# Kernel optimization log

Measured on AMD Instinct MI355X. Metric: run time of the kernel, lower is better.

## Reference

```python
import jax, jax.numpy as jnp
import numpy as np

EPS = 1e-5  # batch-norm epsilon


def subm_conv(feat, nbrs, W):
    # feat: [N, Cin], nbrs: [N, K] int indices into feat (rulebook), W: [K, Cin, Cout]
    gathered = feat[nbrs]                      # [N, K, Cin]  irregular gather
    return jnp.einsum('nkc,kcd->nd', gathered, W)


def batch_norm(f, gamma, beta):
    # training-mode BN over active sites (scn.BatchNormalization semantics)
    mean = jnp.mean(f, axis=0)
    var = jnp.var(f, axis=0)
    return (f - mean) * jax.lax.rsqrt(var + EPS) * gamma + beta


def setup_inputs() -> dict:
    key = jax.random.key(0)
    k1, k2, k3, k4 = jax.random.split(key, 4)
    N, K, C = 300000, 9, 64
    scale = 1.0 / np.sqrt(K * C)
    return {
        'x': jax.random.normal(k1, (N, C), dtype=jnp.float32),
        'nbrs': jax.random.randint(k2, (N, K), 0, N, dtype=jnp.int32),
        'W1': jax.random.normal(k3, (K, C, C), dtype=jnp.float32) * scale,
        'gamma1': jnp.ones((C,), jnp.float32),
        'beta1': jnp.zeros((C,), jnp.float32),
        'W2': jax.random.normal(k4, (K, C, C), dtype=jnp.float32) * scale,
        'gamma2': jnp.ones((C,), jnp.float32),
        'beta2': jnp.zeros((C,), jnp.float32),
    }


def reference(x, nbrs, W1, gamma1, beta1, W2, gamma2, beta2):
    residual = x
    out = subm_conv(x, nbrs, W1)                       # conv1 (no bias)
    out = jax.nn.relu(batch_norm(out, gamma1, beta1))  # BatchNormReLU
    out = subm_conv(out, nbrs, W2)                     # conv2 (no bias)
    out = batch_norm(out, gamma2, beta2)               # BatchNormalization
    out = jax.nn.relu(out + residual)                  # AddTable + ReLU
    return out
```

## Files before the change

### kernel.cpp

```cpp
#include <hip/hip_runtime.h>

#define NROWS 300000
#define NBLK ((NROWS + 63) / 64)

typedef float f32x4 __attribute__((ext_vector_type(4)));
typedef short s16x8 __attribute__((ext_vector_type(8)));
typedef unsigned short u16x8 __attribute__((ext_vector_type(8)));
typedef unsigned short u16x4 __attribute__((ext_vector_type(4)));

__device__ __forceinline__ float bf2f(unsigned short u) {
    return __uint_as_float(((unsigned)u) << 16);
}
__device__ __forceinline__ unsigned short f2bf(float f) {
    unsigned u = __float_as_uint(f);
    u += 0x7FFFu + ((u >> 16) & 1u);
    return (unsigned short)(u >> 16);
}

__global__ __launch_bounds__(256) void x2bf(const float* __restrict__ x,
                                            unsigned short* __restrict__ xb) {
    const int NQ = NROWS * 8;
    for (int i = blockIdx.x * 256 + threadIdx.x; i < NQ; i += gridDim.x * 256) {
        const float4 v0 = *(const float4*)(x + (size_t)i * 8);
        const float4 v1 = *(const float4*)(x + (size_t)i * 8 + 4);
        u16x8 o;
        o[0] = f2bf(v0.x); o[1] = f2bf(v0.y); o[2] = f2bf(v0.z); o[3] = f2bf(v0.w);
        o[4] = f2bf(v1.x); o[5] = f2bf(v1.y); o[6] = f2bf(v1.z); o[7] = f2bf(v1.w);
        *(u16x8*)(xb + (size_t)i * 8) = o;
    }
}

__global__ __launch_bounds__(256) void w_prep(const float* __restrict__ W1,
                                              const float* __restrict__ W2,
                                              unsigned short* __restrict__ WT1,
                                              unsigned short* __restrict__ WT2) {
    const int i = blockIdx.x * 256 + threadIdx.x;
    if (i < 9 * 4096) {
        const int k = i >> 12, cc = (i >> 6) & 63, d = i & 63;
        const int o = k * 4096 + d * 64 + cc;
        WT1[o] = f2bf(W1[i]);
        WT2[o] = f2bf(W2[i]);
    }
}

__global__ __launch_bounds__(256) void conv_mfma(const unsigned short* __restrict__ xb,
                                                 const int* __restrict__ nbrs,
                                                 const unsigned short* __restrict__ WT,
                                                 unsigned short* __restrict__ outb) {
    const int tid = threadIdx.x;
    const int l = tid & 63;
    const int w = tid >> 6;
    const int lr = l & 15;
    const int kg = l >> 4;
    const int c00 = kg * 8;

    const int rowA = blockIdx.x * 64 + w * 16 + lr;
    const int rowAc = rowA < NROWS ? rowA : NROWS - 1;

    int nb[9];
#pragma unroll
    for (int k = 0; k < 9; ++k) nb[k] = nbrs[rowAc * 9 + k];

    s16x8 raw0[9], raw1[9];
#pragma unroll
    for (int k = 0; k < 9; ++k) {
        const unsigned short* rp = xb + (size_t)nb[k] * 64 + c00;
        raw0[k] = *(const s16x8*)rp;
        raw1[k] = *(const s16x8*)(rp + 32);
    }
#pragma unroll
    for (int k = 0; k < 9; ++k) {
        asm volatile("" :: "v"(raw0[k]), "v"(raw1[k]));
    }

    f32x4 acc[4];
#pragma unroll
    for (int d = 0; d < 4; ++d) {
        acc[d][0] = 0.f; acc[d][1] = 0.f; acc[d][2] = 0.f; acc[d][3] = 0.f;
    }

#pragma unroll
    for (int k = 0; k < 9; ++k) {
        const unsigned short* wp = WT + k * 4096 + lr * 64 + c00;
#pragma unroll
        for (int dj = 0; dj < 4; ++dj) {
            const s16x8 b0 = *(const s16x8*)(wp + dj * 1024);
            const s16x8 b1 = *(const s16x8*)(wp + dj * 1024 + 32);
            acc[dj] = __builtin_amdgcn_mfma_f32_16x16x32_bf16(raw0[k], b0, acc[dj], 0, 0, 0);
            acc[dj] = __builtin_amdgcn_mfma_f32_16x16x32_bf16(raw1[k], b1, acc[dj], 0, 0, 0);
        }
    }

    const int orow0 = blockIdx.x * 64 + w * 16 + kg * 4;
#pragma unroll
    for (int dj = 0; dj < 4; ++dj) {
#pragma unroll
        for (int r = 0; r < 4; ++r) {
            const int orow = orow0 + r;
            if (orow < NROWS) outb[(size_t)orow * 64 + dj * 16 + lr] = f2bf(acc[dj][r]);
        }
    }
}

__global__ __launch_bounds__(256) void bn_stats(const unsigned short* __restrict__ fb,
                                                float* __restrict__ S) {
    const int t = threadIdx.x;
    const int c4 = (t & 15) * 4;
    const int rg = t >> 4;
    float s0 = 0, s1 = 0, s2 = 0, s3 = 0, q0 = 0, q1 = 0, q2 = 0, q3 = 0;
    for (int r = blockIdx.x * 16 + rg; r < NROWS; r += gridDim.x * 16) {
        const u16x4 v = *(const u16x4*)(fb + (size_t)r * 64 + c4);
        const float f0 = bf2f(v[0]), f1 = bf2f(v[1]), f2 = bf2f(v[2]), f3 = bf2f(v[3]);
        s0 += f0; s1 += f1; s2 += f2; s3 += f3;
        q0 += f0 * f0; q1 += f1 * f1; q2 += f2 * f2; q3 += f3 * f3;
    }
    __shared__ float red[16][64];
    red[rg][c4 + 0] = s0; red[rg][c4 + 1] = s1; red[rg][c4 + 2] = s2; red[rg][c4 + 3] = s3;
    __syncthreads();
    if (t < 64) {
        float a = 0;
#pragma unroll
        for (int i = 0; i < 16; ++i) a += red[i][t];
        atomicAdd(&S[t], a);
    }
    __syncthreads();
    red[rg][c4 + 0] = q0; red[rg][c4 + 1] = q1; red[rg][c4 + 2] = q2; red[rg][c4 + 3] = q3;
    __syncthreads();
    if (t < 64) {
        float a = 0;
#pragma unroll
        for (int i = 0; i < 16; ++i) a += red[i][t];
        atomicAdd(&S[64 + t], a);
    }
}

__global__ void bn_finalize(const float* __restrict__ S, const float* __restrict__ gamma,
                            const float* __restrict__ beta, float* __restrict__ sb) {
    const int c = threadIdx.x;
    if (c < 64) {
        const float mean = S[c] * (1.0f / NROWS);
        const float var = S[64 + c] * (1.0f / NROWS) - mean * mean;
        const float sc = gamma[c] * rsqrtf(var + 1e-5f);
        sb[c] = sc;
        sb[64 + c] = beta[c] - mean * sc;
    }
}

__global__ __launch_bounds__(256) void bn_apply(unsigned short* __restrict__ fb,
                                                const float* __restrict__ sb) {
    const int NQ = NROWS * 8;
    for (int i = blockIdx.x * 256 + threadIdx.x; i < NQ; i += gridDim.x * 256) {
        const int c8 = (i & 7) * 8;
        u16x8 v = *(const u16x8*)(fb + (size_t)i * 8);
        u16x8 o;
#pragma unroll
        for (int j = 0; j < 8; ++j) {
            const float f = fmaxf(bf2f(v[j]) * sb[c8 + j] + sb[64 + c8 + j], 0.f);
            o[j] = f2bf(f);
        }
        *(u16x8*)(fb + (size_t)i * 8) = o;
    }
}

__global__ __launch_bounds__(256) void final_out(const unsigned short* __restrict__ o2,
                                                 const float* __restrict__ x,
                                                 const float* __restrict__ sb,
                                                 float* __restrict__ out) {
    const int NQ = NROWS * 16;
    for (int i = blockIdx.x * 256 + threadIdx.x; i < NQ; i += gridDim.x * 256) {
        const int c4 = (i & 15) * 4;
        const u16x4 v = *(const u16x4*)(o2 + (size_t)i * 4);
        const float4 xv = *(const float4*)(x + (size_t)i * 4);
        const float4 s = *(const float4*)(sb + c4);
        const float4 b = *(const float4*)(sb + 64 + c4);
        float4 o;
        o.x = fmaxf(bf2f(v[0]) * s.x + b.x + xv.x, 0.f);
        o.y = fmaxf(bf2f(v[1]) * s.y + b.y + xv.y, 0.f);
        o.z = fmaxf(bf2f(v[2]) * s.z + b.z + xv.z, 0.f);
        o.w = fmaxf(bf2f(v[3]) * s.w + b.w + xv.w, 0.f);
        *(float4*)(out + (size_t)i * 4) = o;
    }
}

extern "C" void kernel_launch(void* const* d_in, const int* in_sizes, int n_in,
                              void* d_out, int out_size, void* d_ws, size_t ws_size,
                              hipStream_t stream) {
    const float* x      = (const float*)d_in[0];
    const int*   nbrs   = (const int*)d_in[1];
    const float* W1     = (const float*)d_in[2];
    const float* gamma1 = (const float*)d_in[3];
    const float* beta1  = (const float*)d_in[4];
    const float* W2     = (const float*)d_in[5];
    const float* gamma2 = (const float*)d_in[6];
    const float* beta2  = (const float*)d_in[7];
    float* out = (float*)d_out;

    char* ws = (char*)d_ws;
    unsigned short* out2b = (unsigned short*)ws;
    unsigned short* WT1   = (unsigned short*)(ws + 38400000);
    unsigned short* WT2   = (unsigned short*)(ws + 38400000 + 73728);
    float* Sa  = (float*)(ws + 38400000 + 147456);
    float* Sb  = Sa + 128;
    float* sb1 = Sa + 256;
    float* sb2 = Sa + 384;
    unsigned short* out1b = (unsigned short*)d_out;
    unsigned short* xb    = (unsigned short*)d_out + 19200000;

    hipMemsetAsync(Sa, 0, 256 * sizeof(float), stream);
    x2bf<<<2048, 256, 0, stream>>>(x, xb);
    w_prep<<<144, 256, 0, stream>>>(W1, W2, WT1, WT2);
    conv_mfma<<<NBLK, 256, 0, stream>>>(xb, nbrs, WT1, out1b);
    bn_stats<<<1024, 256, 0, stream>>>(out1b, Sa);
    bn_finalize<<<1, 64, 0, stream>>>(Sa, gamma1, beta1, sb1);
    bn_apply<<<2048, 256, 0, stream>>>(out1b, sb1);
    conv_mfma<<<NBLK, 256, 0, stream>>>(out1b, nbrs, WT2, out2b);
    bn_stats<<<1024, 256, 0, stream>>>(out2b, Sb);
    bn_finalize<<<1, 64, 0, stream>>>(Sb, gamma2, beta2, sb2);
    final_out<<<2048, 256, 0, stream>>>(out2b, x, sb2, out);
}
```

Before: 524.7 us.

## Fuse BN1+ReLU into conv2 gather and replace atomic stats with partials

The separate bn_apply pass is removed. BN1 scale/shift and ReLU are now applied to the gathered neighbour rows inside the second conv kernel, at the cost of recomputing them 9 times per row. BN statistics are written as per-block partials over 128 blocks and reduced in the finalize kernel, which replaces the atomics and the memset. Nontemporal loads and stores are added to the final output pass and the conv2 output, and the asm register barrier in the conv kernel is dropped.

```diff
diff --git a/kernel.cpp b/kernel.cpp
--- a/kernel.cpp
+++ b/kernel.cpp
@@ -2,6 +2,7 @@
 
 #define NROWS 300000
 #define NBLK ((NROWS + 63) / 64)
+#define NPART 128
 
 typedef float f32x4 __attribute__((ext_vector_type(4)));
 typedef short s16x8 __attribute__((ext_vector_type(8)));
@@ -21,11 +22,11 @@
                                             unsigned short* __restrict__ xb) {
     const int NQ = NROWS * 8;
     for (int i = blockIdx.x * 256 + threadIdx.x; i < NQ; i += gridDim.x * 256) {
-        const float4 v0 = *(const float4*)(x + (size_t)i * 8);
-        const float4 v1 = *(const float4*)(x + (size_t)i * 8 + 4);
+        const f32x4 v0 = *(const f32x4*)(x + (size_t)i * 8);
+        const f32x4 v1 = *(const f32x4*)(x + (size_t)i * 8 + 4);
         u16x8 o;
-        o[0] = f2bf(v0.x); o[1] = f2bf(v0.y); o[2] = f2bf(v0.z); o[3] = f2bf(v0.w);
-        o[4] = f2bf(v1.x); o[5] = f2bf(v1.y); o[6] = f2bf(v1.z); o[7] = f2bf(v1.w);
+        o[0] = f2bf(v0[0]); o[1] = f2bf(v0[1]); o[2] = f2bf(v0[2]); o[3] = f2bf(v0[3]);
+        o[4] = f2bf(v1[0]); o[5] = f2bf(v1[1]); o[6] = f2bf(v1[2]); o[7] = f2bf(v1[3]);
         *(u16x8*)(xb + (size_t)i * 8) = o;
     }
 }
@@ -43,9 +44,11 @@
     }
 }
 
+template <int CONV>
 __global__ __launch_bounds__(256) void conv_mfma(const unsigned short* __restrict__ xb,
                                                  const int* __restrict__ nbrs,
                                                  const unsigned short* __restrict__ WT,
+                                                 const float* __restrict__ sb,
                                                  unsigned short* __restrict__ outb) {
     const int tid = threadIdx.x;
     const int l = tid & 63;
@@ -57,6 +60,15 @@
     const int rowA = blockIdx.x * 64 + w * 16 + lr;
     const int rowAc = rowA < NROWS ? rowA : NROWS - 1;
 
+    float s0r[8], b0r[8], s1r[8], b1r[8];
+    if (CONV == 2) {
+#pragma unroll
+        for (int j = 0; j < 8; ++j) {
+            s0r[j] = sb[c00 + j];       b0r[j] = sb[64 + c00 + j];
+            s1r[j] = sb[32 + c00 + j];  b1r[j] = sb[96 + c00 + j];
+        }
+    }
+
     int nb[9];
 #pragma unroll
     for (int k = 0; k < 9; ++k) nb[k] = nbrs[rowAc * 9 + k];
@@ -68,10 +80,6 @@
         raw0[k] = *(const s16x8*)rp;
         raw1[k] = *(const s16x8*)(rp + 32);
     }
-#pragma unroll
-    for (int k = 0; k < 9; ++k) {
-        asm volatile("" :: "v"(raw0[k]), "v"(raw1[k]));
-    }
 
     f32x4 acc[4];
 #pragma unroll
@@ -81,13 +89,23 @@
 
 #pragma unroll
     for (int k = 0; k < 9; ++k) {
+        s16x8 a0 = raw0[k], a1 = raw1[k];
+        if (CONV == 2) {
+#pragma unroll
+            for (int j = 0; j < 8; ++j) {
+                const float f0 = fmaxf(bf2f((unsigned short)a0[j]) * s0r[j] + b0r[j], 0.f);
+                const float f1 = fmaxf(bf2f((unsigned short)a1[j]) * s1r[j] + b1r[j], 0.f);
+                a0[j] = (short)f2bf(f0);
+                a1[j] = (short)f2bf(f1);
+            }
+        }
         const unsigned short* wp = WT + k * 4096 + lr * 64 + c00;
 #pragma unroll
         for (int dj = 0; dj < 4; ++dj) {
             const s16x8 b0 = *(const s16x8*)(wp + dj * 1024);
             const s16x8 b1 = *(const s16x8*)(wp + dj * 1024 + 32);
-            acc[dj] = __builtin_amdgcn_mfma_f32_16x16x32_bf16(raw0[k], b0, acc[dj], 0, 0, 0);
-            acc[dj] = __builtin_amdgcn_mfma_f32_16x16x32_bf16(raw1[k], b1, acc[dj], 0, 0, 0);
+            acc[dj] = __builtin_amdgcn_mfma_f32_16x16x32_bf16(a0, b0, acc[dj], 0, 0, 0);
+            acc[dj] = __builtin_amdgcn_mfma_f32_16x16x32_bf16(a1, b1, acc[dj], 0, 0, 0);
         }
     }
 
@@ -97,13 +115,19 @@
 #pragma unroll
         for (int r = 0; r < 4; ++r) {
             const int orow = orow0 + r;
-            if (orow < NROWS) outb[(size_t)orow * 64 + dj * 16 + lr] = f2bf(acc[dj][r]);
+            if (orow < NROWS) {
+                const unsigned short bv = f2bf(acc[dj][r]);
+                if (CONV == 2)
+                    __builtin_nontemporal_store(bv, &outb[(size_t)orow * 64 + dj * 16 + lr]);
+                else
+                    outb[(size_t)orow * 64 + dj * 16 + lr] = bv;
+            }
         }
     }
 }
 
 __global__ __launch_bounds__(256) void bn_stats(const unsigned short* __restrict__ fb,
-                                                float* __restrict__ S) {
+                                                float* __restrict__ P) {
     const int t = threadIdx.x;
     const int c4 = (t & 15) * 4;
     const int rg = t >> 4;
@@ -121,7 +145,7 @@
         float a = 0;
 #pragma unroll
         for (int i = 0; i < 16; ++i) a += red[i][t];
-        atomicAdd(&S[t], a);
+        P[blockIdx.x * 128 + t] = a;
     }
     __syncthreads();
     red[rg][c4 + 0] = q0; red[rg][c4 + 1] = q1; red[rg][c4 + 2] = q2; red[rg][c4 + 3] = q3;
@@ -130,35 +154,24 @@
         float a = 0;
 #pragma unroll
         for (int i = 0; i < 16; ++i) a += red[i][t];
-        atomicAdd(&S[64 + t], a);
-    }
-}
-
-__global__ void bn_finalize(const float* __restrict__ S, const float* __restrict__ gamma,
+        P[blockIdx.x * 128 + 64 + t] = a;
+    }
+}
+
+__global__ void bn_finalize(const float* __restrict__ P, const float* __restrict__ gamma,
                             const float* __restrict__ beta, float* __restrict__ sb) {
-    const int c = threadIdx.x;
-    if (c < 64) {
-        const float mean = S[c] * (1.0f / NROWS);
-        const float var = S[64 + c] * (1.0f / NROWS) - mean * mean;
-        const float sc = gamma[c] * rsqrtf(var + 1e-5f);
-        sb[c] = sc;
-        sb[64 + c] = beta[c] - mean * sc;
-    }
-}
-
-__global__ __launch_bounds__(256) void bn_apply(unsigned short* __restrict__ fb,
-                                                const float* __restrict__ sb) {
-    const int NQ = NROWS * 8;
-    for (int i = blockIdx.x * 256 + threadIdx.x; i < NQ; i += gridDim.x * 256) {
-        const int c8 = (i & 7) * 8;
-        u16x8 v = *(const u16x8*)(fb + (size_t)i * 8);
-        u16x8 o;
-#pragma unroll
-        for (int j = 0; j < 8; ++j) {
-            const float f = fmaxf(bf2f(v[j]) * sb[c8 + j] + sb[64 + c8 + j], 0.f);
-            o[j] = f2bf(f);
-        }
-        *(u16x8*)(fb + (size_t)i * 8) = o;
+    __shared__ float tot[128];
+    const int t = threadIdx.x;
+    float a = 0.f;
+    for (int p = 0; p < NPART; ++p) a += P[p * 128 + t];
+    tot[t] = a;
+    __syncthreads();
+    if (t < 64) {
+        const float mean = tot[t] * (1.0f / NROWS);
+        const float var = tot[64 + t] * (1.0f / NROWS) - mean * mean;
+        const float sc = gamma[t] * rsqrtf(var + 1e-5f);
+        sb[t] = sc;
+        sb[64 + t] = beta[t] - mean * sc;
     }
 }
 
@@ -169,16 +182,16 @@
     const int NQ = NROWS * 16;
     for (int i = blockIdx.x * 256 + threadIdx.x; i < NQ; i += gridDim.x * 256) {
         const int c4 = (i & 15) * 4;
-        const u16x4 v = *(const u16x4*)(o2 + (size_t)i * 4);
-        const float4 xv = *(const float4*)(x + (size_t)i * 4);
-        const float4 s = *(const float4*)(sb + c4);
-        const float4 b = *(const float4*)(sb + 64 + c4);
-        float4 o;
-        o.x = fmaxf(bf2f(v[0]) * s.x + b.x + xv.x, 0.f);
-        o.y = fmaxf(bf2f(v[1]) * s.y + b.y + xv.y, 0.f);
-        o.z = fmaxf(bf2f(v[2]) * s.z + b.z + xv.z, 0.f);
-        o.w = fmaxf(bf2f(v[3]) * s.w + b.w + xv.w, 0.f);
-        *(float4*)(out + (size_t)i * 4) = o;
+        const u16x4 v = __builtin_nontemporal_load((const u16x4*)(o2 + (size_t)i * 4));
+        const f32x4 xv = __builtin_nontemporal_load((const f32x4*)(x + (size_t)i * 4));
+        const f32x4 s = *(const f32x4*)(sb + c4);
+        const f32x4 b = *(const f32x4*)(sb + 64 + c4);
+        f32x4 o;
+        o[0] = fmaxf(bf2f(v[0]) * s[0] + b[0] + xv[0], 0.f);
+        o[1] = fmaxf(bf2f(v[1]) * s[1] + b[1] + xv[1], 0.f);
+        o[2] = fmaxf(bf2f(v[2]) * s[2] + b[2] + xv[2], 0.f);
+        o[3] = fmaxf(bf2f(v[3]) * s[3] + b[3] + xv[3], 0.f);
+        __builtin_nontemporal_store(o, (f32x4*)(out + (size_t)i * 4));
     }
 }
 
@@ -199,22 +212,20 @@
     unsigned short* out2b = (unsigned short*)ws;
     unsigned short* WT1   = (unsigned short*)(ws + 38400000);
     unsigned short* WT2   = (unsigned short*)(ws + 38400000 + 73728);
-    float* Sa  = (float*)(ws + 38400000 + 147456);
-    float* Sb  = Sa + 128;
-    float* sb1 = Sa + 256;
-    float* sb2 = Sa + 384;
+    float* P1  = (float*)(ws + 38400000 + 147456);
+    float* P2  = (float*)(ws + 38400000 + 147456 + 65536);
+    float* sb1 = (float*)(ws + 38400000 + 147456 + 131072);
+    float* sb2 = sb1 + 128;
     unsigned short* out1b = (unsigned short*)d_out;
     unsigned short* xb    = (unsigned short*)d_out + 19200000;
 
-    hipMemsetAsync(Sa, 0, 256 * sizeof(float), stream);
     x2bf<<<2048, 256, 0, stream>>>(x, xb);
     w_prep<<<144, 256, 0, stream>>>(W1, W2, WT1, WT2);
-    conv_mfma<<<NBLK, 256, 0, stream>>>(xb, nbrs, WT1, out1b);
-    bn_stats<<<1024, 256, 0, stream>>>(out1b, Sa);
-    bn_finalize<<<1, 64, 0, stream>>>(Sa, gamma1, beta1, sb1);
-    bn_apply<<<2048, 256, 0, stream>>>(out1b, sb1);
-    conv_mfma<<<NBLK, 256, 0, stream>>>(out1b, nbrs, WT2, out2b);
-    bn_stats<<<1024, 256, 0, stream>>>(out2b, Sb);
-    bn_finalize<<<1, 64, 0, stream>>>(Sb, gamma2, beta2, sb2);
+    conv_mfma<1><<<NBLK, 256, 0, stream>>>(xb, nbrs, WT1, nullptr, out1b);
+    bn_stats<<<NPART, 256, 0, stream>>>(out1b, P1);
+    bn_finalize<<<1, 128, 0, stream>>>(P1, gamma1, beta1, sb1);
+    conv_mfma<2><<<NBLK, 256, 0, stream>>>(out1b, nbrs, WT2, sb1, out2b);
+    bn_stats<<<NPART, 256, 0, stream>>>(out2b, P2);
+    bn_finalize<<<1, 128, 0, stream>>>(P2, gamma2, beta2, sb2);
     final_out<<<2048, 256, 0, stream>>>(out2b, x, sb2, out);
 }
```

Result: slower. 558.4 us (+6.4%).
